# Kernel tuning notes

Hardware: AMD Instinct MI355X
Metric: run time of the kernel (lower is better)

## Reference

```python
import jax, jax.numpy as jnp
import numpy as np

B, T, D = 2, 2048, 2048
H, KV, HD, RD = 16, 4, 128, 64  # n_heads, n_kv_heads, head_dim, rope_head_dim
THETA = 10000.0


def setup_inputs() -> dict:
    key = jax.random.key(0)
    ks = jax.random.split(key, 5)
    x = jax.random.normal(ks[0], (B, T, D), dtype=jnp.float32)
    Wq = jax.random.normal(ks[1], (D, H * HD), dtype=jnp.float32) * 0.02
    Wk = jax.random.normal(ks[2], (D, KV * HD), dtype=jnp.float32) * 0.02
    Wv = jax.random.normal(ks[3], (D, KV * HD), dtype=jnp.float32) * 0.02
    Wo = jax.random.normal(ks[4], (H * HD, D), dtype=jnp.float32) * 0.02
    # RoPE frequencies for the first RD dims of each head
    inv_freq = 1.0 / (THETA ** (jnp.arange(0, RD, 2, dtype=jnp.float32) / RD))  # [RD/2]
    ang = jnp.arange(T, dtype=jnp.float32)[:, None] * inv_freq[None, :]         # [T, RD/2]
    return {"x": x, "freqs_cos": jnp.cos(ang), "freqs_sin": jnp.sin(ang),
            "Wq": Wq, "Wk": Wk, "Wv": Wv, "Wo": Wo}


def _apply_rope(t, cos, sin):
    # t: [B, h, T, HD]; rotate first RD dims treating consecutive pairs as complex
    rot = t[..., :RD].reshape(*t.shape[:-1], RD // 2, 2)
    e, o = rot[..., 0], rot[..., 1]
    c = cos[None, None]  # [1,1,T,RD/2]
    s = sin[None, None]
    re = e * c - o * s
    ro = e * s + o * c
    rot_out = jnp.stack([re, ro], axis=-1).reshape(*t.shape[:-1], RD)
    return jnp.concatenate([rot_out, t[..., RD:]], axis=-1)


def reference(x, freqs_cos, freqs_sin, Wq, Wk, Wv, Wo):
    q = (x @ Wq).reshape(B, T, H, HD).transpose(0, 2, 1, 3)   # [B,H,T,HD]
    k = (x @ Wk).reshape(B, T, KV, HD).transpose(0, 2, 1, 3)  # [B,KV,T,HD]
    v = (x @ Wv).reshape(B, T, KV, HD).transpose(0, 2, 1, 3)
    q = _apply_rope(q, freqs_cos, freqs_sin)
    k = _apply_rope(k, freqs_cos, freqs_sin)
    present_k, present_v = k, v
    rep = H // KV
    kr = jnp.repeat(k, rep, axis=1)  # GQA repeat_interleave -> [B,H,T,HD]
    vr = jnp.repeat(v, rep, axis=1)
    scores = jnp.einsum('bhqd,bhkd->bhqk', q, kr) / jnp.sqrt(jnp.asarray(HD, q.dtype))
    causal = jnp.tril(jnp.ones((T, T), dtype=bool))
    scores = jnp.where(causal[None, None], scores, jnp.asarray(-1e9, scores.dtype))
    attn = jax.nn.softmax(scores, axis=-1)
    y = jnp.einsum('bhqk,bhkd->bhqd', attn, vr)
    y = y.transpose(0, 2, 1, 3).reshape(B, T, H * HD) @ Wo  # [B,T,D]
    return y, present_k, present_v
```

## Files before the change

kernel.cpp:

```cpp
#include <hip/hip_runtime.h>
#include <hip/hip_bf16.h>

static constexpr int B_  = 2;
static constexpr int T_  = 2048;
static constexpr int D_  = 2048;
static constexpr int H_  = 16;
static constexpr int KV_ = 4;
static constexpr int HD_ = 128;
static constexpr int RD_ = 64;
static constexpr int BT_ = B_ * T_;
static constexpr int NPROJ_ = 3072;
static constexpr float SCALE_ = 0.08838834764831845f;

typedef __attribute__((ext_vector_type(8))) short bf16x8;
typedef __attribute__((ext_vector_type(8))) unsigned short u16x8;
typedef __attribute__((ext_vector_type(4))) float f32x4;

#define COMPILER_BARRIER() __asm__ __volatile__("" ::: "memory")

typedef const __attribute__((address_space(1))) unsigned int* as1_u32p;
typedef __attribute__((address_space(3))) unsigned int* as3_u32p;
#define GLOAD16(g, l) __builtin_amdgcn_global_load_lds((as1_u32p)(const void*)(g), (as3_u32p)(void*)(l), 16, 0, 0)

__device__ __forceinline__ unsigned short f2bu(float f) {
  unsigned x = __float_as_uint(f);
  unsigned r = (x + 0x7fffu + ((x >> 16) & 1u)) >> 16;
  return (unsigned short)r;
}

__global__ __launch_bounds__(256) void cvt_bf16(const float* __restrict__ in,
                                                unsigned short* __restrict__ out) {
  const size_t i = ((size_t)blockIdx.x * 256 + threadIdx.x) * 4;
  const float4 f = *(const float4*)(in + i);
  ushort4 o;
  o.x = f2bu(f.x); o.y = f2bu(f.y); o.z = f2bu(f.z); o.w = f2bu(f.w);
  *(ushort4*)(out + i) = o;
}

__global__ __launch_bounds__(256) void t32_all(const float* __restrict__ Wq,
                                               const float* __restrict__ Wk,
                                               const float* __restrict__ Wv,
                                               const float* __restrict__ Wo,
                                               unsigned short* __restrict__ Wqt,
                                               unsigned short* __restrict__ Wkvt,
                                               unsigned short* __restrict__ Wot) {
  const float* in; unsigned short* out; int C;
  switch (blockIdx.z) {
    case 0:  in = Wq; out = Wqt;                       C = 2048; break;
    case 1:  in = Wk; out = Wkvt;                      C = 512;  break;
    case 2:  in = Wv; out = Wkvt + (size_t)512 * D_;   C = 512;  break;
    default: in = Wo; out = Wot;                       C = 2048; break;
  }
  if ((int)blockIdx.y * 32 >= C) return;

  __shared__ unsigned short tile[32][36];
  const int r0 = blockIdx.x * 32;
  const int c0 = blockIdx.y * 32;
  const int tid = threadIdx.x;
  {
    const int r = tid >> 3;
    const int c = (tid & 7) * 4;
    const float4 f = *(const float4*)(in + (size_t)(r0 + r) * C + c0 + c);
    ushort4 w;
    w.x = f2bu(f.x); w.y = f2bu(f.y); w.z = f2bu(f.z); w.w = f2bu(f.w);
    *(ushort4*)&tile[r][c] = w;
  }
  __syncthreads();
  {
    const int c = tid >> 3;
    const int r = (tid & 7) * 4;
    ushort4 o;
    o.x = tile[r + 0][c];
    o.y = tile[r + 1][c];
    o.z = tile[r + 2][c];
    o.w = tile[r + 3][c];
    *(ushort4*)(out + (size_t)(c0 + c) * D_ + r0 + r) = o;
  }
}

__global__ __launch_bounds__(256) void gemm_proj(const unsigned short* __restrict__ A,
                                                 const unsigned short* __restrict__ Bt,
                                                 unsigned short* __restrict__ Qbf,
                                                 float* __restrict__ kout,
                                                 float* __restrict__ vout,
                                                 unsigned short* __restrict__ Kbf,
                                                 const float* __restrict__ cosb,
                                                 const float* __restrict__ sinb) {
  __shared__ __align__(16) unsigned short As[128 * 32];
  __shared__ __align__(16) unsigned short Bs[128 * 32];
  const int tid = threadIdx.x;
  const int lane = tid & 63;
  const int wave = tid >> 6;
  const int n16 = lane & 15;
  const int quad = lane >> 4;
  const int bm = blockIdx.y * 128;
  const int bn = blockIdx.x * 128;
  const int wm = (wave & 1) * 64;
  const int wn = (wave >> 1) * 64;
  const int K = D_;

  const int gr = tid >> 2;
  const int gc = (tid & 3) * 8;
  const unsigned short* agA = A  + (size_t)(bm + gr) * K + gc;
  const unsigned short* agB = A  + (size_t)(bm + 64 + gr) * K + gc;
  const unsigned short* bgA = Bt + (size_t)(bn + gr) * K + gc;
  const unsigned short* bgB = Bt + (size_t)(bn + 64 + gr) * K + gc;
  unsigned short* lAs0 = As + wave * 512;
  unsigned short* lAs1 = As + 2048 + wave * 512;
  unsigned short* lBs0 = Bs + wave * 512;
  unsigned short* lBs1 = Bs + 2048 + wave * 512;

  f32x4 acc[4][4];
#pragma unroll
  for (int mi = 0; mi < 4; ++mi)
#pragma unroll
    for (int ni = 0; ni < 4; ++ni) acc[mi][ni] = (f32x4){0.f, 0.f, 0.f, 0.f};

  for (int k0 = 0; k0 < K; k0 += 32) {
    GLOAD16(agA + k0, lAs0);
    GLOAD16(agB + k0, lAs1);
    GLOAD16(bgA + k0, lBs0);
    GLOAD16(bgB + k0, lBs1);
    __syncthreads();

    bf16x8 af[4], bf[4];
#pragma unroll
    for (int i = 0; i < 4; ++i) {
      af[i] = *(const bf16x8*)&As[(wm + i * 16 + n16) * 32 + quad * 8];
      bf[i] = *(const bf16x8*)&Bs[(wn + i * 16 + n16) * 32 + quad * 8];
    }
#pragma unroll
    for (int mi = 0; mi < 4; ++mi)
#pragma unroll
      for (int ni = 0; ni < 4; ++ni)
        acc[mi][ni] = __builtin_amdgcn_mfma_f32_16x16x32_bf16(af[mi], bf[ni], acc[mi][ni], 0, 0, 0);
    __syncthreads();
  }

  const int colbase = bn + wn;
#pragma unroll
  for (int mi = 0; mi < 4; ++mi) {
#pragma unroll
    for (int r = 0; r < 4; ++r) {
      const int row = bm + wm + mi * 16 + quad * 4 + r;
      const int b = row >> 11, t = row & (T_ - 1);
#pragma unroll
      for (int ni = 0; ni < 4; ++ni) {
        const int col = colbase + ni * 16 + n16;
        const int hd = col & 127;
        float v = acc[mi][ni][r];
        const float other = __shfl_xor(v, 1);
        if (col < 2560 && hd < RD_) {
          const float c = cosb[t * 32 + (hd >> 1)];
          const float s = sinb[t * 32 + (hd >> 1)];
          v = (col & 1) ? (other * s + v * c) : (v * c - other * s);
        }
        if (col < 2048) {
          Qbf[(size_t)row * (H_ * HD_) + col] = f2bu(v * SCALE_);
        } else if (col < 2560) {
          const int kv = (col - 2048) >> 7;
          const size_t idx = (((size_t)(b * KV_ + kv) * T_) + t) * HD_ + hd;
          kout[idx] = v;
          Kbf[idx] = f2bu(v);
        } else {
          const int kv = (col - 2560) >> 7;
          vout[(((size_t)(b * KV_ + kv) * T_) + t) * HD_ + hd] = v;
        }
      }
    }
  }
}

__global__ __launch_bounds__(256) void gemm_bf16(const unsigned short* __restrict__ A,
                                                 const unsigned short* __restrict__ Bt,
                                                 float* __restrict__ C,
                                                 int M, int N, int K) {
  __shared__ __align__(16) unsigned short As[128 * 32];
  __shared__ __align__(16) unsigned short Bs[128 * 32];
  const int tid = threadIdx.x;
  const int lane = tid & 63;
  const int wave = tid >> 6;
  const int n16 = lane & 15;
  const int quad = lane >> 4;
  const int bm = blockIdx.y * 128;
  const int bn = blockIdx.x * 128;
  const int wm = (wave & 1) * 64;
  const int wn = (wave >> 1) * 64;

  const int gr = tid >> 2;
  const int gc = (tid & 3) * 8;
  const unsigned short* agA = A  + (size_t)(bm + gr) * K + gc;
  const unsigned short* agB = A  + (size_t)(bm + 64 + gr) * K + gc;
  const unsigned short* bgA = Bt + (size_t)(bn + gr) * K + gc;
  const unsigned short* bgB = Bt + (size_t)(bn + 64 + gr) * K + gc;
  unsigned short* lAs0 = As + wave * 512;
  unsigned short* lAs1 = As + 2048 + wave * 512;
  unsigned short* lBs0 = Bs + wave * 512;
  unsigned short* lBs1 = Bs + 2048 + wave * 512;

  f32x4 acc[4][4];
#pragma unroll
  for (int mi = 0; mi < 4; ++mi)
#pragma unroll
    for (int ni = 0; ni < 4; ++ni) acc[mi][ni] = (f32x4){0.f, 0.f, 0.f, 0.f};

  for (int k0 = 0; k0 < K; k0 += 32) {
    GLOAD16(agA + k0, lAs0);
    GLOAD16(agB + k0, lAs1);
    GLOAD16(bgA + k0, lBs0);
    GLOAD16(bgB + k0, lBs1);
    __syncthreads();

    bf16x8 af[4], bf[4];
#pragma unroll
    for (int i = 0; i < 4; ++i) {
      af[i] = *(const bf16x8*)&As[(wm + i * 16 + n16) * 32 + quad * 8];
      bf[i] = *(const bf16x8*)&Bs[(wn + i * 16 + n16) * 32 + quad * 8];
    }
#pragma unroll
    for (int mi = 0; mi < 4; ++mi)
#pragma unroll
      for (int ni = 0; ni < 4; ++ni)
        acc[mi][ni] = __builtin_amdgcn_mfma_f32_16x16x32_bf16(af[mi], bf[ni], acc[mi][ni], 0, 0, 0);
    __syncthreads();
  }

#pragma unroll
  for (int mi = 0; mi < 4; ++mi) {
#pragma unroll
    for (int r = 0; r < 4; ++r) {
      const int row = bm + wm + mi * 16 + quad * 4 + r;
#pragma unroll
      for (int ni = 0; ni < 4; ++ni) {
        const int col = bn + wn + ni * 16 + n16;
        C[(size_t)row * N + col] = acc[mi][ni][r];
      }
    }
  }
}

__global__ __launch_bounds__(256) void v_transpose(const float* __restrict__ vin,
                                                   unsigned short* __restrict__ vt) {
  __shared__ unsigned int tile[32][17];
  const int tid = threadIdx.x;
  const int k0 = blockIdx.x * 32;
  const int d0 = blockIdx.y * 32;
  const int g  = blockIdx.z;
  const float* src = vin + ((size_t)g * T_ + k0) * HD_ + d0;

  {
    const int kr = tid >> 3;
    const int d2 = (tid & 7) * 2;
#pragma unroll
    for (int c = 0; c < 2; ++c) {
      const float2 f = *(const float2*)(src + (size_t)kr * HD_ + (d2 + c) * 2);
      tile[kr][d2 + c] = (unsigned)f2bu(f.x) | ((unsigned)f2bu(f.y) << 16);
    }
  }
  __syncthreads();
  {
    const int dr = tid >> 3;
    const int kc = (tid & 7) * 4;
    const int dstb = ((kc & 15) << 1) | ((kc & 16) >> 2);
    const int hi = dr >> 1;
    const int sh = (dr & 1) * 16;
    ushort4 o;
    o.x = (unsigned short)(tile[kc + 0][hi] >> sh);
    o.y = (unsigned short)(tile[kc + 1][hi] >> sh);
    o.z = (unsigned short)(tile[kc + 2][hi] >> sh);
    o.w = (unsigned short)(tile[kc + 3][hi] >> sh);
    *(ushort4*)(vt + ((size_t)g * HD_ + d0 + dr) * T_ + k0 + dstb) = o;
  }
}

__global__ __launch_bounds__(256, 2) void attn_flash(const unsigned short* __restrict__ Q,
                                                     const unsigned short* __restrict__ Kbf,
                                                     const unsigned short* __restrict__ VbfT,
                                                     unsigned short* __restrict__ O) {
  __shared__ __align__(16) unsigned short Ks[32 * 128];
  __shared__ __align__(16) unsigned short Vs[128 * 32];

  const int tid = threadIdx.x;
  const int wave = tid >> 6;
  const int lane = tid & 63;
  const int n16 = lane & 15;
  const int quad = lane >> 4;
  const int pid = blockIdx.x;
  const int q0A = pid * 16;
  const int q0B = (127 - pid) * 16;
  const int nchA = (q0A + 47) >> 5;
  const int nchB = (q0B + 47) >> 5;
  const int bkv = blockIdx.y;
  const int b = bkv >> 2;
  const int kvh = bkv & 3;
  const int h = kvh * 4 + wave;

  const unsigned short* ksrc = Kbf + ((size_t)(b * KV_ + kvh)) * T_ * HD_;
  const unsigned short* vtsrc = VbfT + ((size_t)(b * KV_ + kvh)) * HD_ * T_;

  const int krow = tid >> 4;
  const int kcol = (tid & 15) * 8;
  const int kdst0 = (krow * 128 + kcol) ^ ((krow & 7) << 3);
  const int kdst1 = ((krow + 16) * 128 + kcol) ^ ((krow & 7) << 3);
  const int vrow = tid >> 2;
  const int vcol = (tid & 3) * 8;
  const int vdst0 = (vrow * 32 + vcol) ^ ((vrow & 3) << 3);
  const int vdst1 = ((vrow + 64) * 32 + vcol) ^ ((vrow & 3) << 3);

  bf16x8 qfA[4], qfB[4];
  {
    const unsigned short* qa = Q + ((size_t)(b * T_ + q0A + n16)) * (H_ * HD_) + h * HD_ + quad * 8;
    const unsigned short* qb = Q + ((size_t)(b * T_ + q0B + n16)) * (H_ * HD_) + h * HD_ + quad * 8;
#pragma unroll
    for (int s = 0; s < 4; ++s) {
      qfA[s] = *(const bf16x8*)(qa + s * 32);
      qfB[s] = *(const bf16x8*)(qb + s * 32);
    }
  }

  float mA = -1e30f, lA = 0.f;
  float mB = -1e30f, lB = 0.f;
  f32x4 oA[8], oB[8];
#pragma unroll
  for (int t = 0; t < 8; ++t) { oA[t] = (f32x4){0.f,0.f,0.f,0.f}; oB[t] = (f32x4){0.f,0.f,0.f,0.f}; }

  {
    const u16x8 ka = *(const u16x8*)(ksrc + (size_t)krow * HD_ + kcol);
    const u16x8 kb = *(const u16x8*)(ksrc + (size_t)(krow + 16) * HD_ + kcol);
    const u16x8 va = *(const u16x8*)(vtsrc + (size_t)vrow * T_ + vcol);
    const u16x8 vb = *(const u16x8*)(vtsrc + (size_t)(vrow + 64) * T_ + vcol);
    *(u16x8*)&Ks[kdst0] = ka;
    *(u16x8*)&Ks[kdst1] = kb;
    *(u16x8*)&Vs[vdst0] = va;
    *(u16x8*)&Vs[vdst1] = vb;
  }
  __syncthreads();

  for (int c = 0; c < nchB; ++c) {
    const int kc = c * 32;
    const bool actA = (c < nchA);

    u16x8 ka, kb, va, vb;
    if (c + 1 < nchB) {
      ka = *(const u16x8*)(ksrc + (size_t)(kc + 32 + krow) * HD_ + kcol);
      kb = *(const u16x8*)(ksrc + (size_t)(kc + 48 + krow) * HD_ + kcol);
      va = *(const u16x8*)(vtsrc + (size_t)vrow * T_ + (kc + 32) + vcol);
      vb = *(const u16x8*)(vtsrc + (size_t)(vrow + 64) * T_ + (kc + 32) + vcol);
    }
    COMPILER_BARRIER();

    f32x4 sB0 = (f32x4){0.f,0.f,0.f,0.f}, sB1 = sB0, sA0 = sB0, sA1 = sB0;
#pragma unroll
    for (int s = 0; s < 4; ++s) {
      const bf16x8 kf0 = *(const bf16x8*)&Ks[(n16 * 128 + quad * 8 + s * 32) ^ ((n16 & 7) << 3)];
      const bf16x8 kf1 = *(const bf16x8*)&Ks[((16 + n16) * 128 + quad * 8 + s * 32) ^ ((n16 & 7) << 3)];
      sB0 = __builtin_amdgcn_mfma_f32_16x16x32_bf16(kf0, qfB[s], sB0, 0, 0, 0);
      sB1 = __builtin_amdgcn_mfma_f32_16x16x32_bf16(kf1, qfB[s], sB1, 0, 0, 0);
      if (actA) {
        sA0 = __builtin_amdgcn_mfma_f32_16x16x32_bf16(kf0, qfA[s], sA0, 0, 0, 0);
        sA1 = __builtin_amdgcn_mfma_f32_16x16x32_bf16(kf1, qfA[s], sA1, 0, 0, 0);
      }
    }

    union { bf16x8 v; unsigned short u[8]; } pkB, pkA;
    bool growB;
    float alphaB = 1.f, alphaA = 1.f;
    {
      float s[8];
#pragma unroll
      for (int r = 0; r < 4; ++r) { s[r] = sB0[r]; s[r + 4] = sB1[r]; }
      if (c == nchB - 1) {
        const int qrow = q0B + n16;
#pragma unroll
        for (int r = 0; r < 4; ++r) {
          if (kc + quad * 4 + r > qrow)      s[r]     = -1e30f;
          if (kc + 16 + quad * 4 + r > qrow) s[r + 4] = -1e30f;
        }
      }
      float mm = fmaxf(fmaxf(fmaxf(s[0], s[1]), fmaxf(s[2], s[3])),
                       fmaxf(fmaxf(s[4], s[5]), fmaxf(s[6], s[7])));
      mm = fmaxf(mm, __shfl_xor(mm, 16));
      mm = fmaxf(mm, __shfl_xor(mm, 32));
      growB = __any(mm > mB);
      if (growB) {
        const float mnew = fmaxf(mB, mm);
        alphaB = __expf(mB - mnew);
        mB = mnew;
      }
      float lsum = 0.f;
#pragma unroll
      for (int j = 0; j < 8; ++j) {
        const float p = __expf(s[j] - mB);
        lsum += p;
        pkB.u[j] = f2bu(p);
      }
      lsum += __shfl_xor(lsum, 16);
      lsum += __shfl_xor(lsum, 32);
      lB = growB ? (alphaB * lB + lsum) : (lB + lsum);
    }

    bool growA = false;
    if (actA) {
      float s[8];
#pragma unroll
      for (int r = 0; r < 4; ++r) { s[r] = sA0[r]; s[r + 4] = sA1[r]; }
      if (c == nchA - 1) {
        const int qrow = q0A + n16;
#pragma unroll
        for (int r = 0; r < 4; ++r) {
          if (kc + quad * 4 + r > qrow)      s[r]     = -1e30f;
          if (kc + 16 + quad * 4 + r > qrow) s[r + 4] = -1e30f;
        }
      }
      float mm = fmaxf(fmaxf(fmaxf(s[0], s[1]), fmaxf(s[2], s[3])),
                       fmaxf(fmaxf(s[4], s[5]), fmaxf(s[6], s[7])));
      mm = fmaxf(mm, __shfl_xor(mm, 16));
      mm = fmaxf(mm, __shfl_xor(mm, 32));
      growA = __any(mm > mA);
      if (growA) {
        const float mnew = fmaxf(mA, mm);
        alphaA = __expf(mA - mnew);
        mA = mnew;
      }
      float lsum = 0.f;
#pragma unroll
      for (int j = 0; j < 8; ++j) {
        const float p = __expf(s[j] - mA);
        lsum += p;
        pkA.u[j] = f2bu(p);
      }
      lsum += __shfl_xor(lsum, 16);
      lsum += __shfl_xor(lsum, 32);
      lA = growA ? (alphaA * lA + lsum) : (lA + lsum);
    }

    if (growB) {
      f32x4 av;
#pragma unroll
      for (int r = 0; r < 4; ++r) av[r] = __shfl(alphaB, quad * 4 + r);
#pragma unroll
      for (int t = 0; t < 8; ++t) {
        oB[t][0] *= av[0]; oB[t][1] *= av[1]; oB[t][2] *= av[2]; oB[t][3] *= av[3];
      }
    }
    if (growA) {
      f32x4 av;
#pragma unroll
      for (int r = 0; r < 4; ++r) av[r] = __shfl(alphaA, quad * 4 + r);
#pragma unroll
      for (int t = 0; t < 8; ++t) {
        oA[t][0] *= av[0]; oA[t][1] *= av[1]; oA[t][2] *= av[2]; oA[t][3] *= av[3];
      }
    }

#pragma unroll
    for (int t = 0; t < 8; ++t) {
      const bf16x8 vf = *(const bf16x8*)&Vs[((t * 16 + n16) * 32 + quad * 8) ^ ((n16 & 3) << 3)];
      oB[t] = __builtin_amdgcn_mfma_f32_16x16x32_bf16(pkB.v, vf, oB[t], 0, 0, 0);
      if (actA) oA[t] = __builtin_amdgcn_mfma_f32_16x16x32_bf16(pkA.v, vf, oA[t], 0, 0, 0);
    }

    __syncthreads();
    if (c + 1 < nchB) {
      *(u16x8*)&Ks[kdst0] = ka;
      *(u16x8*)&Ks[kdst1] = kb;
      *(u16x8*)&Vs[vdst0] = va;
      *(u16x8*)&Vs[vdst1] = vb;
    }
    __syncthreads();
  }

  {
    unsigned short* obB = O + ((size_t)(b * T_ + q0B)) * (H_ * HD_) + h * HD_;
    unsigned short* obA = O + ((size_t)(b * T_ + q0A)) * (H_ * HD_) + h * HD_;
#pragma unroll
    for (int r = 0; r < 4; ++r) {
      const float liB = 1.0f / __shfl(lB, quad * 4 + r);
      const float liA = 1.0f / __shfl(lA, quad * 4 + r);
#pragma unroll
      for (int t = 0; t < 8; ++t) {
        obB[(size_t)(quad * 4 + r) * (H_ * HD_) + t * 16 + n16] = f2bu(oB[t][r] * liB);
        obA[(size_t)(quad * 4 + r) * (H_ * HD_) + t * 16 + n16] = f2bu(oA[t][r] * liA);
      }
    }
  }
}

extern "C" void kernel_launch(void* const* d_in, const int* in_sizes, int n_in,
                              void* d_out, int out_size, void* d_ws, size_t ws_size,
                              hipStream_t stream) {
  const float* x  = (const float*)d_in[0];
  const float* fc = (const float*)d_in[1];
  const float* fs = (const float*)d_in[2];
  const float* Wq = (const float*)d_in[3];
  const float* Wk = (const float*)d_in[4];
  const float* Wv = (const float*)d_in[5];
  const float* Wo = (const float*)d_in[6];

  float* yout = (float*)d_out;
  float* kout = yout + (size_t)B_ * T_ * D_;
  float* vout = kout + (size_t)B_ * KV_ * T_ * HD_;
  unsigned short* Qbf = (unsigned short*)yout;

  unsigned short* xb   = (unsigned short*)d_ws;
  unsigned short* Abf  = xb;
  unsigned short* Wqt  = xb   + (size_t)BT_ * D_;
  unsigned short* Wkvt = Wqt  + (size_t)D_ * D_;
  unsigned short* Wot  = Wkvt + (size_t)1024 * D_;
  unsigned short* Kbf  = Wot  + (size_t)D_ * D_;
  unsigned short* VbfT = Kbf  + (size_t)B_ * KV_ * T_ * HD_;

  dim3 blk(256);

  cvt_bf16<<<dim3((BT_ * D_) / 1024), blk, 0, stream>>>(x, xb);
  t32_all<<<dim3(D_ / 32, D_ / 32, 4), blk, 0, stream>>>(Wq, Wk, Wv, Wo, Wqt, Wkvt, Wot);

  gemm_proj<<<dim3(NPROJ_ / 128, BT_ / 128), blk, 0, stream>>>(xb, Wqt, Qbf, kout, vout, Kbf, fc, fs);

  v_transpose<<<dim3(T_ / 32, HD_ / 32, B_ * KV_), blk, 0, stream>>>(vout, VbfT);

  attn_flash<<<dim3(64, B_ * KV_), blk, 0, stream>>>(Qbf, Kbf, VbfT, Abf);

  gemm_bf16<<<dim3(D_ / 128, BT_ / 128), blk, 0, stream>>>(Abf, Wot, yout, BT_, D_, D_);
}
```

Measured before the change: 405.2 us.

## Replace projection GEMMs with 256x256 double-buffered swizzled MFMA kernel

```diff
diff --git a/kernel.cpp b/kernel.cpp
--- a/kernel.cpp
+++ b/kernel.cpp
@@ -17,6 +17,7 @@
 typedef __attribute__((ext_vector_type(4))) float f32x4;
 
 #define COMPILER_BARRIER() __asm__ __volatile__("" ::: "memory")
+#define BAR() do { COMPILER_BARRIER(); __builtin_amdgcn_s_barrier(); COMPILER_BARRIER(); } while (0)
 
 typedef const __attribute__((address_space(1))) unsigned int* as1_u32p;
 typedef __attribute__((address_space(3))) unsigned int* as3_u32p;
@@ -78,165 +79,177 @@
   }
 }
 
-__global__ __launch_bounds__(256) void gemm_proj(const unsigned short* __restrict__ A,
-                                                 const unsigned short* __restrict__ Bt,
-                                                 unsigned short* __restrict__ Qbf,
-                                                 float* __restrict__ kout,
-                                                 float* __restrict__ vout,
-                                                 unsigned short* __restrict__ Kbf,
-                                                 const float* __restrict__ cosb,
-                                                 const float* __restrict__ sinb) {
-  __shared__ __align__(16) unsigned short As[128 * 32];
-  __shared__ __align__(16) unsigned short Bs[128 * 32];
+template <int EPI>
+__global__ __launch_bounds__(512, 1) void gemm256(const unsigned short* __restrict__ A,
+                                                  const unsigned short* __restrict__ Bt,
+                                                  float* __restrict__ C,
+                                                  unsigned short* __restrict__ Qbf,
+                                                  float* __restrict__ kout,
+                                                  float* __restrict__ vout,
+                                                  unsigned short* __restrict__ Kbf,
+                                                  const float* __restrict__ cosb,
+                                                  const float* __restrict__ sinb,
+                                                  int N) {
+  __shared__ __align__(16) unsigned short As[2][256 * 64];
+  __shared__ __align__(16) unsigned short Bs[2][256 * 64];
+  constexpr int K = D_;
+  constexpr int KT = K / 64;
+
   const int tid = threadIdx.x;
   const int lane = tid & 63;
   const int wave = tid >> 6;
   const int n16 = lane & 15;
   const int quad = lane >> 4;
-  const int bm = blockIdx.y * 128;
-  const int bn = blockIdx.x * 128;
-  const int wm = (wave & 1) * 64;
-  const int wn = (wave >> 1) * 64;
-  const int K = D_;
-
-  const int gr = tid >> 2;
-  const int gc = (tid & 3) * 8;
-  const unsigned short* agA = A  + (size_t)(bm + gr) * K + gc;
-  const unsigned short* agB = A  + (size_t)(bm + 64 + gr) * K + gc;
-  const unsigned short* bgA = Bt + (size_t)(bn + gr) * K + gc;
-  const unsigned short* bgB = Bt + (size_t)(bn + 64 + gr) * K + gc;
-  unsigned short* lAs0 = As + wave * 512;
-  unsigned short* lAs1 = As + 2048 + wave * 512;
-  unsigned short* lBs0 = Bs + wave * 512;
-  unsigned short* lBs1 = Bs + 2048 + wave * 512;
-
-  f32x4 acc[4][4];
-#pragma unroll
-  for (int mi = 0; mi < 4; ++mi)
+  const int wm = wave >> 2;
+  const int wn = wave & 3;
+
+  const int nwg = gridDim.x * gridDim.y;
+  int bid = blockIdx.y * gridDim.x + blockIdx.x;
+  bid = (bid & 7) * (nwg >> 3) + (bid >> 3);
+  const int bn = (bid % (int)gridDim.x) * 256;
+  const int bm = (bid / (int)gridDim.x) * 256;
+
+  const int t8 = tid >> 3;
+  const int kg = ((tid & 7) ^ (t8 & 7)) << 3;
+  const unsigned short *aS0[2], *aS1[2], *bS0[2], *bS1[2];
+#pragma unroll
+  for (int g = 0; g < 2; ++g) {
+    aS0[g] = A + (size_t)(bm + g * 128 + t8) * K + kg;
+    aS1[g] = A + (size_t)(bm + g * 128 + 64 + t8) * K + kg;
+    const int br = (g * 2 + (t8 >> 5)) * 64 + (t8 & 31);
+    bS0[g] = Bt + (size_t)(bn + br) * K + kg;
+    bS1[g] = Bt + (size_t)(bn + br + 32) * K + kg;
+  }
+
+#define STAGE(dst, half, src, koff)                                             \
+  do {                                                                          \
+    GLOAD16((src)[0] + (koff), &(dst)[((half) * 128 + 0) * 64 + wave * 512]);   \
+    GLOAD16((src)[1] + (koff), &(dst)[((half) * 128 + 64) * 64 + wave * 512]);  \
+  } while (0)
+
+#define LDA(MH)                                                                   \
+  _Pragma("unroll") for (int ks = 0; ks < 2; ++ks)                                \
+  _Pragma("unroll") for (int i = 0; i < 4; ++i)                                   \
+      aF[ks][i] = *(const bf16x8*)&cA[((MH) * 128 + wm * 64 + i * 16 + n16) * 64  \
+                                      + ((quad * 8 + ks * 32) ^ ((n16 & 7) << 3))];
+
+#define LDB(DST, NH)                                                              \
+  _Pragma("unroll") for (int ks = 0; ks < 2; ++ks)                                \
+  _Pragma("unroll") for (int jj = 0; jj < 2; ++jj)                                \
+      DST[ks][jj] = *(const bf16x8*)&cB[((NH) * 128 + wn * 32 + jj * 16 + n16) * 64 \
+                                        + ((quad * 8 + ks * 32) ^ ((n16 & 7) << 3))];
+
+#define MFQ(MH, NH, BF)                                                           \
+  do {                                                                            \
+    __builtin_amdgcn_s_setprio(1);                                                \
+    _Pragma("unroll") for (int ks = 0; ks < 2; ++ks)                              \
+    _Pragma("unroll") for (int i = 0; i < 4; ++i)                                 \
+    _Pragma("unroll") for (int jj = 0; jj < 2; ++jj)                              \
+        acc[(MH) * 4 + i][(NH) * 2 + jj] = __builtin_amdgcn_mfma_f32_16x16x32_bf16( \
+            aF[ks][i], BF[ks][jj], acc[(MH) * 4 + i][(NH) * 2 + jj], 0, 0, 0);    \
+    __builtin_amdgcn_s_setprio(0);                                                \
+  } while (0)
+
+  f32x4 acc[8][4];
+#pragma unroll
+  for (int mi = 0; mi < 8; ++mi)
 #pragma unroll
     for (int ni = 0; ni < 4; ++ni) acc[mi][ni] = (f32x4){0.f, 0.f, 0.f, 0.f};
 
-  for (int k0 = 0; k0 < K; k0 += 32) {
-    GLOAD16(agA + k0, lAs0);
-    GLOAD16(agB + k0, lAs1);
-    GLOAD16(bgA + k0, lBs0);
-    GLOAD16(bgB + k0, lBs1);
-    __syncthreads();
-
-    bf16x8 af[4], bf[4];
-#pragma unroll
-    for (int i = 0; i < 4; ++i) {
-      af[i] = *(const bf16x8*)&As[(wm + i * 16 + n16) * 32 + quad * 8];
-      bf[i] = *(const bf16x8*)&Bs[(wn + i * 16 + n16) * 32 + quad * 8];
-    }
-#pragma unroll
-    for (int mi = 0; mi < 4; ++mi)
-#pragma unroll
-      for (int ni = 0; ni < 4; ++ni)
-        acc[mi][ni] = __builtin_amdgcn_mfma_f32_16x16x32_bf16(af[mi], bf[ni], acc[mi][ni], 0, 0, 0);
-    __syncthreads();
-  }
-
-  const int colbase = bn + wn;
-#pragma unroll
-  for (int mi = 0; mi < 4; ++mi) {
-#pragma unroll
-    for (int r = 0; r < 4; ++r) {
-      const int row = bm + wm + mi * 16 + quad * 4 + r;
-      const int b = row >> 11, t = row & (T_ - 1);
-#pragma unroll
-      for (int ni = 0; ni < 4; ++ni) {
-        const int col = colbase + ni * 16 + n16;
-        const int hd = col & 127;
-        float v = acc[mi][ni][r];
-        const float other = __shfl_xor(v, 1);
-        if (col < 2560 && hd < RD_) {
-          const float c = cosb[t * 32 + (hd >> 1)];
-          const float s = sinb[t * 32 + (hd >> 1)];
-          v = (col & 1) ? (other * s + v * c) : (v * c - other * s);
+  bf16x8 aF[2][4], b0F[2][2], b1F[2][2];
+
+  STAGE(As[0], 0, aS0, 0);
+  STAGE(Bs[0], 0, bS0, 0);
+  STAGE(Bs[0], 1, bS1, 0);
+  STAGE(As[0], 1, aS1, 0);
+
+  for (int kt = 0; kt < KT - 1; ++kt) {
+    const unsigned short* cA = As[kt & 1];
+    const unsigned short* cB = Bs[kt & 1];
+    unsigned short* nA = As[(kt & 1) ^ 1];
+    unsigned short* nB = Bs[(kt & 1) ^ 1];
+    const int ko = (kt + 1) * 64;
+
+    STAGE(nA, 0, aS0, ko);
+    asm volatile("s_waitcnt vmcnt(6)" ::: "memory");
+    BAR();
+    LDA(0); LDB(b0F, 0);
+    MFQ(0, 0, b0F);
+    STAGE(nB, 0, bS0, ko);
+    asm volatile("s_waitcnt vmcnt(6)" ::: "memory");
+    BAR();
+    LDB(b1F, 1);
+    MFQ(0, 1, b1F);
+    STAGE(nB, 1, bS1, ko);
+    asm volatile("s_waitcnt vmcnt(6)" ::: "memory");
+    BAR();
+    LDA(1);
+    MFQ(1, 0, b0F);
+    STAGE(nA, 1, aS1, ko);
+    MFQ(1, 1, b1F);
+  }
+
+  {
+    const unsigned short* cA = As[(KT - 1) & 1];
+    const unsigned short* cB = Bs[(KT - 1) & 1];
+    asm volatile("s_waitcnt vmcnt(4)" ::: "memory");
+    BAR();
+    LDA(0); LDB(b0F, 0);
+    MFQ(0, 0, b0F);
+    asm volatile("s_waitcnt vmcnt(2)" ::: "memory");
+    BAR();
+    LDB(b1F, 1);
+    MFQ(0, 1, b1F);
+    asm volatile("s_waitcnt vmcnt(0)" ::: "memory");
+    BAR();
+    LDA(1);
+    MFQ(1, 0, b0F);
+    MFQ(1, 1, b1F);
+  }
+
+#pragma unroll
+  for (int mi = 0; mi < 8; ++mi) {
+#pragma unroll
+    for (int rr = 0; rr < 4; ++rr) {
+      const int row = bm + wm * 128 + mi * 16 + quad * 4 + rr;
+      if (EPI == 0) {
+#pragma unroll
+        for (int ni = 0; ni < 4; ++ni) {
+          const int col = bn + wn * 64 + ni * 16 + n16;
+          C[(size_t)row * N + col] = acc[mi][ni][rr];
         }
-        if (col < 2048) {
-          Qbf[(size_t)row * (H_ * HD_) + col] = f2bu(v * SCALE_);
-        } else if (col < 2560) {
-          const int kv = (col - 2048) >> 7;
-          const size_t idx = (((size_t)(b * KV_ + kv) * T_) + t) * HD_ + hd;
-          kout[idx] = v;
-          Kbf[idx] = f2bu(v);
-        } else {
-          const int kv = (col - 2560) >> 7;
-          vout[(((size_t)(b * KV_ + kv) * T_) + t) * HD_ + hd] = v;
+      } else {
+        const int b = row >> 11, t = row & (T_ - 1);
+#pragma unroll
+        for (int ni = 0; ni < 4; ++ni) {
+          const int col = bn + wn * 64 + ni * 16 + n16;
+          const int hd = col & 127;
+          float v = acc[mi][ni][rr];
+          const float other = __shfl_xor(v, 1);
+          if (col < 2560 && hd < RD_) {
+            const float c = cosb[t * 32 + (hd >> 1)];
+            const float s = sinb[t * 32 + (hd >> 1)];
+            v = (col & 1) ? (other * s + v * c) : (v * c - other * s);
+          }
+          if (col < 2048) {
+            Qbf[(size_t)row * (H_ * HD_) + col] = f2bu(v * SCALE_);
+          } else if (col < 2560) {
+            const int kv = (col - 2048) >> 7;
+            const size_t idx = (((size_t)(b * KV_ + kv) * T_) + t) * HD_ + hd;
+            kout[idx] = v;
+            Kbf[idx] = f2bu(v);
+          } else {
+            const int kv = (col - 2560) >> 7;
+            vout[(((size_t)(b * KV_ + kv) * T_) + t) * HD_ + hd] = v;
+          }
         }
       }
     }
   }
-}
-
-__global__ __launch_bounds__(256) void gemm_bf16(const unsigned short* __restrict__ A,
-                                                 const unsigned short* __restrict__ Bt,
-                                                 float* __restrict__ C,
-                                                 int M, int N, int K) {
-  __shared__ __align__(16) unsigned short As[128 * 32];
-  __shared__ __align__(16) unsigned short Bs[128 * 32];
-  const int tid = threadIdx.x;
-  const int lane = tid & 63;
-  const int wave = tid >> 6;
-  const int n16 = lane & 15;
-  const int quad = lane >> 4;
-  const int bm = blockIdx.y * 128;
-  const int bn = blockIdx.x * 128;
-  const int wm = (wave & 1) * 64;
-  const int wn = (wave >> 1) * 64;
-
-  const int gr = tid >> 2;
-  const int gc = (tid & 3) * 8;
-  const unsigned short* agA = A  + (size_t)(bm + gr) * K + gc;
-  const unsigned short* agB = A  + (size_t)(bm + 64 + gr) * K + gc;
-  const unsigned short* bgA = Bt + (size_t)(bn + gr) * K + gc;
-  const unsigned short* bgB = Bt + (size_t)(bn + 64 + gr) * K + gc;
-  unsigned short* lAs0 = As + wave * 512;
-  unsigned short* lAs1 = As + 2048 + wave * 512;
-  unsigned short* lBs0 = Bs + wave * 512;
-  unsigned short* lBs1 = Bs + 2048 + wave * 512;
-
-  f32x4 acc[4][4];
-#pragma unroll
-  for (int mi = 0; mi < 4; ++mi)
-#pragma unroll
-    for (int ni = 0; ni < 4; ++ni) acc[mi][ni] = (f32x4){0.f, 0.f, 0.f, 0.f};
-
-  for (int k0 = 0; k0 < K; k0 += 32) {
-    GLOAD16(agA + k0, lAs0);
-    GLOAD16(agB + k0, lAs1);
-    GLOAD16(bgA + k0, lBs0);
-    GLOAD16(bgB + k0, lBs1);
-    __syncthreads();
-
-    bf16x8 af[4], bf[4];
-#pragma unroll
-    for (int i = 0; i < 4; ++i) {
-      af[i] = *(const bf16x8*)&As[(wm + i * 16 + n16) * 32 + quad * 8];
-      bf[i] = *(const bf16x8*)&Bs[(wn + i * 16 + n16) * 32 + quad * 8];
-    }
-#pragma unroll
-    for (int mi = 0; mi < 4; ++mi)
-#pragma unroll
-      for (int ni = 0; ni < 4; ++ni)
-        acc[mi][ni] = __builtin_amdgcn_mfma_f32_16x16x32_bf16(af[mi], bf[ni], acc[mi][ni], 0, 0, 0);
-    __syncthreads();
-  }
-
-#pragma unroll
-  for (int mi = 0; mi < 4; ++mi) {
-#pragma unroll
-    for (int r = 0; r < 4; ++r) {
-      const int row = bm + wm + mi * 16 + quad * 4 + r;
-#pragma unroll
-      for (int ni = 0; ni < 4; ++ni) {
-        const int col = bn + wn + ni * 16 + n16;
-        C[(size_t)row * N + col] = acc[mi][ni][r];
-      }
-    }
-  }
+#undef STAGE
+#undef LDA
+#undef LDB
+#undef MFQ
 }
 
 __global__ __launch_bounds__(256) void v_transpose(const float* __restrict__ vin,
@@ -515,11 +528,13 @@
   cvt_bf16<<<dim3((BT_ * D_) / 1024), blk, 0, stream>>>(x, xb);
   t32_all<<<dim3(D_ / 32, D_ / 32, 4), blk, 0, stream>>>(Wq, Wk, Wv, Wo, Wqt, Wkvt, Wot);
 
-  gemm_proj<<<dim3(NPROJ_ / 128, BT_ / 128), blk, 0, stream>>>(xb, Wqt, Qbf, kout, vout, Kbf, fc, fs);
+  gemm256<1><<<dim3(NPROJ_ / 256, BT_ / 256), dim3(512), 0, stream>>>(
+      xb, Wqt, nullptr, Qbf, kout, vout, Kbf, fc, fs, NPROJ_);
 
   v_transpose<<<dim3(T_ / 32, HD_ / 32, B_ * KV_), blk, 0, stream>>>(vout, VbfT);
 
   attn_flash<<<dim3(64, B_ * KV_), blk, 0, stream>>>(Qbf, Kbf, VbfT, Abf);
 
-  gemm_bf16<<<dim3(D_ / 128, BT_ / 128), blk, 0, stream>>>(Abf, Wot, yout, BT_, D_, D_);
-}
+  gemm256<0><<<dim3(D_ / 256, BT_ / 256), dim3(512), 0, stream>>>(
+      Abf, Wot, yout, nullptr, nullptr, nullptr, nullptr, nullptr, nullptr, D_);
+}
```

Result: faster. 379.9 us (-6.2%).
